# Kernel optimization log

Measured on AMD Instinct MI355X. Metric: run time of the kernel, lower is better.

The kernel has to match this reference:

```python
import jax, jax.numpy as jnp
import numpy as np
import math

B, S, D, H = 2, 2048, 1024, 32
HD = D // H  # head_dim = 32
NEG = -1e9


def setup_inputs() -> dict:
    key = jax.random.key(0)
    ks = jax.random.split(key, 6)
    x = jax.random.normal(ks[0], (B, S, D), dtype=jnp.float32)
    # additive causal mask: 0 on/below diagonal, -1e9 above
    causal = jnp.tril(jnp.ones((S, S), dtype=bool))
    mask = jnp.where(causal, 0.0, NEG).astype(jnp.float32)[None, None]
    # SSMax-style per-query-position log-length scale
    section_log_len = jnp.log(jnp.arange(1, S + 1, dtype=jnp.float32) + 1.0).reshape(1, 1, S, 1)
    sc = 1.0 / math.sqrt(D)
    wq = jax.random.normal(ks[1], (D, D), dtype=jnp.float32) * sc
    wk = jax.random.normal(ks[2], (D, D), dtype=jnp.float32) * sc
    wv = jax.random.normal(ks[3], (D, D), dtype=jnp.float32) * sc
    wo = jax.random.normal(ks[4], (D, D), dtype=jnp.float32) * sc
    seq_scale = jnp.ones((1, H, 1, 1), dtype=jnp.float32)
    return {"x": x, "mask": mask, "section_log_len": section_log_len,
            "wq": wq, "wk": wk, "wv": wv, "wo": wo, "seq_scale": seq_scale}


def reference(x, mask, section_log_len, wq, wk, wv, wo, seq_scale):
    bsz, seqlen, dim = x.shape
    # projections (torch Linear: y = x @ W.T); split heads -> [b, h, s, hd]
    q = (x @ wq.T).reshape(bsz, seqlen, H, HD).transpose(0, 2, 1, 3)
    k = (x @ wk.T).reshape(bsz, seqlen, H, HD).transpose(0, 2, 1, 3)
    v = (x @ wv.T).reshape(bsz, seqlen, H, HD).transpose(0, 2, 1, 3)
    # n_kv_heads == n_heads, so repeat_kv is identity
    scores = jnp.einsum('bhqd,bhkd->bhqk', q, k) / math.sqrt(HD)
    scores = scores * (section_log_len * seq_scale)  # SSMax per-head learned scale
    scores = scores + mask
    probs = jax.nn.softmax(scores.astype(jnp.float32), axis=-1).astype(q.dtype)
    out = jnp.einsum('bhqk,bhkd->bhqd', probs, v)
    out = out.transpose(0, 2, 1, 3).reshape(bsz, seqlen, dim)
    return out @ wo.T
```

## Files before the change

kernel.cpp:

```cpp
#include <hip/hip_runtime.h>
#include <hip/hip_bf16.h>

typedef __bf16 bf16_t;
typedef bf16_t bf16x8 __attribute__((ext_vector_type(8)));
typedef float f32x4 __attribute__((ext_vector_type(4)));

#define NB 2
#define SEQ 2048
#define DIM 1024
#define NH 32
#define HDIM 32

#define LDA 40

static __device__ __forceinline__ f32x4 mfma16(bf16x8 a, bf16x8 b, f32x4 c) {
    return __builtin_amdgcn_mfma_f32_16x16x32_bf16(a, b, c, 0, 0, 0);
}

static __device__ __forceinline__ void load_lds16(const bf16_t* g, bf16_t* l) {
    __builtin_amdgcn_global_load_lds(
        (const __attribute__((address_space(1))) void*)(g),
        (__attribute__((address_space(3))) void*)(l), 16, 0, 0);
}

__global__ __launch_bounds__(256)
void cvt_f32_bf16(const float* __restrict__ s0, bf16_t* __restrict__ d0, int n0,
                  const float* __restrict__ s1, bf16_t* __restrict__ d1, int n1,
                  const float* __restrict__ s2, bf16_t* __restrict__ d2, int n2,
                  const float* __restrict__ s3, bf16_t* __restrict__ d3, int n3,
                  const float* __restrict__ s4, bf16_t* __restrict__ d4, int n4) {
    const int stride = gridDim.x * blockDim.x;
    const int tid = blockIdx.x * blockDim.x + threadIdx.x;
    const float* src[5] = {s0, s1, s2, s3, s4};
    bf16_t* dst[5] = {d0, d1, d2, d3, d4};
    const int n[5] = {n0, n1, n2, n3, n4};
#pragma unroll
    for (int r = 0; r < 5; r++) {
        const int nv = n[r] >> 2;
        for (int i = tid; i < nv; i += stride) {
            float4 v = ((const float4*)src[r])[i];
            bf16_t o[4] = {(bf16_t)v.x, (bf16_t)v.y, (bf16_t)v.z, (bf16_t)v.w};
            *(uint2*)(dst[r] + i * 4) = *(const uint2*)o;
        }
    }
}

template <int EPI, int BM>
__global__ __launch_bounds__(256)
void gemm_pipe(const bf16_t* __restrict__ A, const bf16_t* __restrict__ W,
               float* __restrict__ Cf, bf16_t* __restrict__ qb,
               bf16_t* __restrict__ kb, bf16_t* __restrict__ vtb,
               const float* __restrict__ slen, const float* __restrict__ ss) {
    constexpr int MI = BM / 32;
    __shared__ alignas(16) bf16_t As[2 * BM * 32];
    __shared__ alignas(16) bf16_t Bs[2 * 128 * 32];
    const int t = threadIdx.x;
    const int lane = t & 63, wave = t >> 6;
    const int lane16 = lane & 15, quad = lane >> 4;
    const int wm = (wave >> 1) * (BM / 2), wn = (wave & 1) * 64;
    const int id = blockIdx.x;
    int m0, n0g;
    if (EPI == 1) {
        const int xcd = id & 7, slot = id >> 3;
        m0 = (xcd + 8 * (slot & 3)) * 128;
        n0g = (slot >> 2) * 128;
    } else {
        const int xcd = id & 7, slot = id >> 3;
        m0 = (xcd + 8 * (slot & 7)) * 64;
        n0g = (slot >> 3) * 128;
    }
    const int tr = t >> 2;
    const int tc = (t & 3) * 8;
    const bf16_t* ga = A + (m0 + tr) * DIM + tc;
    const bf16_t* gb = W + (n0g + tr) * DIM + tc;
    const bool vseg = (EPI == 1) && (n0g >= 2048);

    f32x4 acc[MI][4];
#pragma unroll
    for (int i = 0; i < MI; i++)
#pragma unroll
        for (int j = 0; j < 4; j++) acc[i][j] = f32x4{0.f, 0.f, 0.f, 0.f};

    auto stage = [&](int k0, int buf) {
        bf16_t* a_dst = As + buf * (BM * 32) + (t & 192) * 8;
        bf16_t* b_dst = Bs + buf * 4096 + (t & 192) * 8;
        load_lds16(ga + k0, a_dst);
        if (BM == 128) load_lds16(ga + 64 * DIM + k0, a_dst + 2048);
        load_lds16(gb + k0, b_dst);
        load_lds16(gb + 64 * DIM + k0, b_dst + 2048);
    };
    auto compute = [&](int buf) {
        bf16x8 af[MI], bfr[4];
#pragma unroll
        for (int mi = 0; mi < MI; mi++)
            af[mi] = *(const bf16x8*)(As + buf * (BM * 32) +
                                      (wm + mi * 16 + lane16) * 32 + quad * 8);
#pragma unroll
        for (int ni = 0; ni < 4; ni++)
            bfr[ni] = *(const bf16x8*)(Bs + buf * 4096 +
                                       (wn + ni * 16 + lane16) * 32 + quad * 8);
        if (vseg) {
#pragma unroll
            for (int mi = 0; mi < MI; mi++)
#pragma unroll
                for (int ni = 0; ni < 4; ni++)
                    acc[mi][ni] = mfma16(bfr[ni], af[mi], acc[mi][ni]);
        } else {
#pragma unroll
            for (int mi = 0; mi < MI; mi++)
#pragma unroll
                for (int ni = 0; ni < 4; ni++)
                    acc[mi][ni] = mfma16(af[mi], bfr[ni], acc[mi][ni]);
        }
    };

    stage(0, 0);
#pragma unroll
    for (int k0 = 0; k0 < DIM; k0 += 32) {
        const int cur = (k0 >> 5) & 1;
        if (k0 + 32 < DIM) {
            stage(k0 + 32, cur ^ 1);
            if (BM == 128)
                asm volatile("s_waitcnt vmcnt(4)" ::: "memory");
            else
                asm volatile("s_waitcnt vmcnt(3)" ::: "memory");
        } else {
            asm volatile("s_waitcnt vmcnt(0)" ::: "memory");
        }
        asm volatile("s_barrier" ::: "memory");
        compute(cur);
        if (k0 + 32 < DIM) {
            asm volatile("s_waitcnt lgkmcnt(0)" ::: "memory");
            asm volatile("s_barrier" ::: "memory");
        }
    }

    if (EPI == 0) {
#pragma unroll
        for (int mi = 0; mi < MI; mi++)
#pragma unroll
            for (int ni = 0; ni < 4; ni++)
#pragma unroll
                for (int r = 0; r < 4; r++) {
                    int row = m0 + wm + mi * 16 + quad * 4 + r;
                    int col = n0g + wn + ni * 16 + lane16;
                    Cf[row * DIM + col] = acc[mi][ni][r];
                }
    } else if (!vseg) {
        const bool isq = (n0g < 1024);
        bf16_t* dst = isq ? qb : kb;
        const int nb = n0g & 1023;
#pragma unroll
        for (int mi = 0; mi < MI; mi++)
#pragma unroll
            for (int ni = 0; ni < 4; ni++) {
                const int h = ((nb + wn) >> 5) + (ni >> 1);
                const float hscale =
                    isq ? ss[h] * 0.17677669529663687f : 0.f;
#pragma unroll
                for (int r = 0; r < 4; r++) {
                    int m = m0 + wm + mi * 16 + quad * 4 + r;
                    int nl = nb + wn + ni * 16 + lane16;
                    int b = m >> 11, s = m & (SEQ - 1);
                    int d = nl & 31;
                    float v = acc[mi][ni][r];
                    if (isq) v *= slen[s] * hscale;
                    dst[(((b * NH + h) << 11) + s) * 32 + d] = (bf16_t)v;
                }
            }
    } else {
        const int nb = n0g & 1023;
#pragma unroll
        for (int mi = 0; mi < MI; mi++)
#pragma unroll
            for (int ni = 0; ni < 4; ni++)
#pragma unroll
                for (int r = 0; r < 4; r++) {
                    int nl = nb + wn + ni * 16 + quad * 4 + r;
                    int m = m0 + wm + mi * 16 + lane16;
                    int b = m >> 11, s = m & (SEQ - 1);
                    int h = nl >> 5, d = nl & 31;
                    vtb[(((b * NH + h) << 5) + d) * SEQ + s] = (bf16_t)acc[mi][ni][r];
                }
    }
}

__global__ __launch_bounds__(256)
void attn_fwd(const bf16_t* __restrict__ q, const bf16_t* __restrict__ k,
              const bf16_t* __restrict__ vt, bf16_t* __restrict__ out) {
    __shared__ alignas(16) bf16_t pscr[4][32 * LDA];
    const int t = threadIdx.x;
    const int lane = t & 63, wave = t >> 6;
    const int lane16 = lane & 15, quad = lane >> 4;
    const int gw = blockIdx.x * 4 + wave;
    const int idx = gw & 63;
    const int qt = (idx & 1) ? (63 - (idx >> 1)) : (idx >> 1);
    const int h = (gw >> 6) & (NH - 1);
    const int b = gw >> 11;
    const int q0 = qt * 32;
    const bf16_t* qh = q + (b * NH + h) * SEQ * HDIM;
    const bf16_t* kh = k + (b * NH + h) * SEQ * HDIM;
    const bf16_t* vth = vt + (b * NH + h) * HDIM * SEQ;
    bf16_t* psw = pscr[wave];

    bf16x8 qf[2];
    qf[0] = *(const bf16x8*)(qh + (q0 + lane16) * HDIM + quad * 8);
    qf[1] = *(const bf16x8*)(qh + (q0 + 16 + lane16) * HDIM + quad * 8);

    f32x4 o[2][2];
    float lrow[2][4];
#pragma unroll
    for (int mi = 0; mi < 2; mi++)
#pragma unroll
        for (int r = 0; r < 4; r++) lrow[mi][r] = 0.f;
#pragma unroll
    for (int mi = 0; mi < 2; mi++)
#pragma unroll
        for (int ni = 0; ni < 2; ni++) o[mi][ni] = f32x4{0.f, 0.f, 0.f, 0.f};

    const bf16_t* kp0 = kh + (2 * lane16) * HDIM + quad * 8;
    const bf16_t* vp0 = vth + lane16 * SEQ + quad * 8;
    const bf16_t* vp1 = vth + (16 + lane16) * SEQ + quad * 8;

    auto process = [&](bf16x8 kf0, bf16x8 kf1, int kv, bool domask) {
        const f32x4 zz = f32x4{0.f, 0.f, 0.f, 0.f};
        f32x4 sc[2][2];
        sc[0][0] = mfma16(qf[0], kf0, zz);
        sc[0][1] = mfma16(qf[0], kf1, zz);
        sc[1][0] = mfma16(qf[1], kf0, zz);
        sc[1][1] = mfma16(qf[1], kf1, zz);
        bf16x8 vf0 = *(const bf16x8*)(vp0 + kv);
        bf16x8 vf1 = *(const bf16x8*)(vp1 + kv);
#pragma unroll
        for (int mi = 0; mi < 2; mi++)
#pragma unroll
            for (int r = 0; r < 4; r++) {
                float p0 = __expf(sc[mi][0][r]);
                float p1 = __expf(sc[mi][1][r]);
                if (domask) {
                    const int rowloc = mi * 16 + quad * 4 + r;
                    if (2 * lane16 > rowloc) p0 = 0.f;
                    if (2 * lane16 + 1 > rowloc) p1 = 0.f;
                }
                lrow[mi][r] += p0 + p1;
                bf16_t pb[2] = {(bf16_t)p0, (bf16_t)p1};
                *(unsigned int*)(psw + (mi * 16 + quad * 4 + r) * LDA +
                                 2 * lane16) = *(const unsigned int*)pb;
            }
        asm volatile("s_waitcnt lgkmcnt(0)" ::: "memory");
        bf16x8 pf0 = *(const bf16x8*)(psw + lane16 * LDA + quad * 8);
        bf16x8 pf1 = *(const bf16x8*)(psw + (16 + lane16) * LDA + quad * 8);
        o[0][0] = mfma16(pf0, vf0, o[0][0]);
        o[0][1] = mfma16(pf0, vf1, o[0][1]);
        o[1][0] = mfma16(pf1, vf0, o[1][0]);
        o[1][1] = mfma16(pf1, vf1, o[1][1]);
    };

    bf16x8 kc0 = *(const bf16x8*)(kp0);
    bf16x8 kc1 = *(const bf16x8*)(kp0 + HDIM);
    for (int kv = 0; kv < q0; kv += 32) {
        bf16x8 kn0 = *(const bf16x8*)(kp0 + (kv + 32) * HDIM);
        bf16x8 kn1 = *(const bf16x8*)(kp0 + (kv + 32) * HDIM + HDIM);
        process(kc0, kc1, kv, false);
        kc0 = kn0;
        kc1 = kn1;
    }
    process(kc0, kc1, q0, true);

#pragma unroll
    for (int mi = 0; mi < 2; mi++)
#pragma unroll
        for (int r = 0; r < 4; r++) {
            float l = lrow[mi][r];
#pragma unroll
            for (int off = 1; off < 16; off <<= 1) l += __shfl_xor(l, off);
            float inv = 1.0f / l;
            int qi = q0 + mi * 16 + quad * 4 + r;
            bf16_t* ob = out + (b * SEQ + qi) * DIM + h * HDIM;
#pragma unroll
            for (int ni = 0; ni < 2; ni++)
                ob[ni * 16 + lane16] = (bf16_t)(o[mi][ni][r] * inv);
        }
}

extern "C" void kernel_launch(void* const* d_in, const int* in_sizes, int n_in,
                              void* d_out, int out_size, void* d_ws, size_t ws_size,
                              hipStream_t stream) {
    const float* x = (const float*)d_in[0];
    const float* slen = (const float*)d_in[2];
    const float* wq = (const float*)d_in[3];
    const float* wk = (const float*)d_in[4];
    const float* wv = (const float*)d_in[5];
    const float* wo = (const float*)d_in[6];
    const float* ss = (const float*)d_in[7];

    const size_t ELEMS = (size_t)NB * SEQ * DIM;
    const size_t WELEMS = (size_t)DIM * DIM;
    bf16_t* xb = (bf16_t*)d_ws;
    bf16_t* abuf = xb;
    bf16_t* wqkvb = xb + ELEMS;
    bf16_t* wob = wqkvb + 3 * WELEMS;
    bf16_t* qbuf = wob + WELEMS;
    bf16_t* vtbuf = qbuf + ELEMS;
    bf16_t* kbuf = (bf16_t*)d_out;

    dim3 blk(256);
    cvt_f32_bf16<<<dim3(1024), blk, 0, stream>>>(
        x, xb, (int)ELEMS, wq, wqkvb, (int)WELEMS, wk, wqkvb + WELEMS,
        (int)WELEMS, wv, wqkvb + 2 * WELEMS, (int)WELEMS, wo, wob, (int)WELEMS);

    gemm_pipe<1, 128><<<dim3(768), blk, 0, stream>>>(
        xb, wqkvb, nullptr, qbuf, kbuf, vtbuf, slen, ss);
    attn_fwd<<<dim3(NB * NH * (SEQ / 32) / 4), blk, 0, stream>>>(
        qbuf, kbuf, vtbuf, abuf);
    gemm_pipe<0, 64><<<dim3(512), blk, 0, stream>>>(
        abuf, wob, (float*)d_out, nullptr, nullptr, nullptr, nullptr, nullptr);
}
```

Baseline: 214.0 us.

## Split attention KV range across wave pairs, use exp2 with folded log2e scale

Each query tile is now handled by two waves that split the causal KV range in half and combine their partial outputs and row sums through shared memory, which doubles the grid and shortens the longest per-wave loop. The log2(e) factor is folded into the Q scaling so the softmax can use the raw v_exp_f32 instruction instead of __expf. s_setprio is raised around the MFMA blocks to favour matrix issue. The cost is an extra block-wide barrier and an LDS reduction, and half the waves sit idle during the final normalisation.

```diff
diff --git a/kernel.cpp b/kernel.cpp
--- a/kernel.cpp
+++ b/kernel.cpp
@@ -15,6 +15,12 @@
 
 static __device__ __forceinline__ f32x4 mfma16(bf16x8 a, bf16x8 b, f32x4 c) {
     return __builtin_amdgcn_mfma_f32_16x16x32_bf16(a, b, c, 0, 0, 0);
+}
+
+static __device__ __forceinline__ float fexp2(float x) {
+    float r;
+    asm("v_exp_f32 %0, %1" : "=v"(r) : "v"(x));
+    return r;
 }
 
 static __device__ __forceinline__ void load_lds16(const bf16_t* g, bf16_t* l) {
@@ -156,7 +162,8 @@
             for (int ni = 0; ni < 4; ni++) {
                 const int h = ((nb + wn) >> 5) + (ni >> 1);
                 const float hscale =
-                    isq ? ss[h] * 0.17677669529663687f : 0.f;
+                    isq ? ss[h] * (0.17677669529663687f * 1.4426950408889634f)
+                        : 0.f;
 #pragma unroll
                 for (int r = 0; r < 4; r++) {
                     int m = m0 + wm + mi * 16 + quad * 4 + r;
@@ -189,14 +196,16 @@
 void attn_fwd(const bf16_t* __restrict__ q, const bf16_t* __restrict__ k,
               const bf16_t* __restrict__ vt, bf16_t* __restrict__ out) {
     __shared__ alignas(16) bf16_t pscr[4][32 * LDA];
+    __shared__ float comb[2][64][25];
     const int t = threadIdx.x;
     const int lane = t & 63, wave = t >> 6;
     const int lane16 = lane & 15, quad = lane >> 4;
-    const int gw = blockIdx.x * 4 + wave;
-    const int idx = gw & 63;
-    const int qt = (idx & 1) ? (63 - (idx >> 1)) : (idx >> 1);
-    const int h = (gw >> 6) & (NH - 1);
-    const int b = gw >> 11;
+    const int pairid = wave >> 1;
+    const int whalf = wave & 1;
+    const int s0i = blockIdx.x >> 6;
+    const int bh = blockIdx.x & 63;
+    const int h = bh & (NH - 1), b = bh >> 5;
+    const int qt = 63 - 2 * s0i - pairid;
     const int q0 = qt * 32;
     const bf16_t* qh = q + (b * NH + h) * SEQ * HDIM;
     const bf16_t* kh = k + (b * NH + h) * SEQ * HDIM;
@@ -225,18 +234,20 @@
     auto process = [&](bf16x8 kf0, bf16x8 kf1, int kv, bool domask) {
         const f32x4 zz = f32x4{0.f, 0.f, 0.f, 0.f};
         f32x4 sc[2][2];
+        __builtin_amdgcn_s_setprio(1);
         sc[0][0] = mfma16(qf[0], kf0, zz);
         sc[0][1] = mfma16(qf[0], kf1, zz);
         sc[1][0] = mfma16(qf[1], kf0, zz);
         sc[1][1] = mfma16(qf[1], kf1, zz);
+        __builtin_amdgcn_s_setprio(0);
         bf16x8 vf0 = *(const bf16x8*)(vp0 + kv);
         bf16x8 vf1 = *(const bf16x8*)(vp1 + kv);
 #pragma unroll
         for (int mi = 0; mi < 2; mi++)
 #pragma unroll
             for (int r = 0; r < 4; r++) {
-                float p0 = __expf(sc[mi][0][r]);
-                float p1 = __expf(sc[mi][1][r]);
+                float p0 = fexp2(sc[mi][0][r]);
+                float p1 = fexp2(sc[mi][1][r]);
                 if (domask) {
                     const int rowloc = mi * 16 + quad * 4 + r;
                     if (2 * lane16 > rowloc) p0 = 0.f;
@@ -250,22 +261,60 @@
         asm volatile("s_waitcnt lgkmcnt(0)" ::: "memory");
         bf16x8 pf0 = *(const bf16x8*)(psw + lane16 * LDA + quad * 8);
         bf16x8 pf1 = *(const bf16x8*)(psw + (16 + lane16) * LDA + quad * 8);
+        __builtin_amdgcn_s_setprio(1);
         o[0][0] = mfma16(pf0, vf0, o[0][0]);
         o[0][1] = mfma16(pf0, vf1, o[0][1]);
         o[1][0] = mfma16(pf1, vf0, o[1][0]);
         o[1][1] = mfma16(pf1, vf1, o[1][1]);
+        __builtin_amdgcn_s_setprio(0);
     };
 
-    bf16x8 kc0 = *(const bf16x8*)(kp0);
-    bf16x8 kc1 = *(const bf16x8*)(kp0 + HDIM);
-    for (int kv = 0; kv < q0; kv += 32) {
-        bf16x8 kn0 = *(const bf16x8*)(kp0 + (kv + 32) * HDIM);
-        bf16x8 kn1 = *(const bf16x8*)(kp0 + (kv + 32) * HDIM + HDIM);
-        process(kc0, kc1, kv, false);
-        kc0 = kn0;
-        kc1 = kn1;
-    }
-    process(kc0, kc1, q0, true);
+    const int nh = (qt + 1) >> 1;
+    const int kvb = whalf ? 0 : nh * 32;
+    const int kve = whalf ? nh * 32 - 32 : q0;
+    if (kve >= kvb) {
+        bf16x8 kc0 = *(const bf16x8*)(kp0 + kvb * HDIM);
+        bf16x8 kc1 = *(const bf16x8*)(kp0 + kvb * HDIM + HDIM);
+        for (int kv = kvb; kv < kve; kv += 32) {
+            bf16x8 kn0 = *(const bf16x8*)(kp0 + (kv + 32) * HDIM);
+            bf16x8 kn1 = *(const bf16x8*)(kp0 + (kv + 32) * HDIM + HDIM);
+            process(kc0, kc1, kv, false);
+            kc0 = kn0;
+            kc1 = kn1;
+        }
+        process(kc0, kc1, kve, kve == q0);
+    }
+
+    if (whalf) {
+        float* c = comb[pairid][lane];
+#pragma unroll
+        for (int mi = 0; mi < 2; mi++)
+#pragma unroll
+            for (int ni = 0; ni < 2; ni++)
+#pragma unroll
+                for (int r = 0; r < 4; r++)
+                    c[(mi * 2 + ni) * 4 + r] = o[mi][ni][r];
+#pragma unroll
+        for (int mi = 0; mi < 2; mi++)
+#pragma unroll
+            for (int r = 0; r < 4; r++) c[16 + mi * 4 + r] = lrow[mi][r];
+    }
+    __syncthreads();
+    if (whalf) return;
+    {
+        const float* c = comb[pairid][lane];
+#pragma unroll
+        for (int mi = 0; mi < 2; mi++)
+#pragma unroll
+            for (int ni = 0; ni < 2; ni++)
+#pragma unroll
+                for (int r = 0; r < 4; r++)
+                    o[mi][ni][r] += c[(mi * 2 + ni) * 4 + r];
+#pragma unroll
+        for (int mi = 0; mi < 2; mi++)
+#pragma unroll
+            for (int r = 0; r < 4; r++) lrow[mi][r] += c[16 + mi * 4 + r];
+    }
 
 #pragma unroll
     for (int mi = 0; mi < 2; mi++)
@@ -311,7 +360,7 @@
 
     gemm_pipe<1, 128><<<dim3(768), blk, 0, stream>>>(
         xb, wqkvb, nullptr, qbuf, kbuf, vtbuf, slen, ss);
-    attn_fwd<<<dim3(NB * NH * (SEQ / 32) / 4), blk, 0, stream>>>(
+    attn_fwd<<<dim3(NB * NH * (SEQ / 32) / 2), blk, 0, stream>>>(
         qbuf, kbuf, vtbuf, abuf);
     gemm_pipe<0, 64><<<dim3(512), blk, 0, stream>>>(
         abuf, wob, (float*)d_out, nullptr, nullptr, nullptr, nullptr, nullptr);
```

Result: slower. 219.7 us (+2.7%).

## Software-pipeline attention loop with double-buffered P scratch and MFMA row sums

Applied to the files above, without the earlier changes.

Restructures the attention inner loop so the QK MFMAs for block i overlap with the exp and LDS write for block i and the PV MFMAs for block i-1, using two LDS P buffers per wave. This removes the explicit lgkmcnt wait between writing and reading P. Row sums are now computed by an MFMA against a ones vector instead of scalar adds plus a shuffle reduction. exp is done with a raw v_exp_f32 (base 2), with log2(e) folded into the Q scale, and s_setprio hints are placed around the MFMA groups. Without the explicit wait, LDS ordering relies on the compiler's own waitcnt insertion, and the row sums now come from bf16-rounded probabilities.

```diff
diff --git a/kernel.cpp b/kernel.cpp
--- a/kernel.cpp
+++ b/kernel.cpp
@@ -15,6 +15,12 @@
 
 static __device__ __forceinline__ f32x4 mfma16(bf16x8 a, bf16x8 b, f32x4 c) {
     return __builtin_amdgcn_mfma_f32_16x16x32_bf16(a, b, c, 0, 0, 0);
+}
+
+static __device__ __forceinline__ float fexp2(float x) {
+    float r;
+    asm("v_exp_f32 %0, %1" : "=v"(r) : "v"(x));
+    return r;
 }
 
 static __device__ __forceinline__ void load_lds16(const bf16_t* g, bf16_t* l) {
@@ -156,7 +162,8 @@
             for (int ni = 0; ni < 4; ni++) {
                 const int h = ((nb + wn) >> 5) + (ni >> 1);
                 const float hscale =
-                    isq ? ss[h] * 0.17677669529663687f : 0.f;
+                    isq ? ss[h] * (0.17677669529663687f * 1.4426950408889634f)
+                        : 0.f;
 #pragma unroll
                 for (int r = 0; r < 4; r++) {
                     int m = m0 + wm + mi * 16 + quad * 4 + r;
@@ -188,7 +195,7 @@
 __global__ __launch_bounds__(256)
 void attn_fwd(const bf16_t* __restrict__ q, const bf16_t* __restrict__ k,
               const bf16_t* __restrict__ vt, bf16_t* __restrict__ out) {
-    __shared__ alignas(16) bf16_t pscr[4][32 * LDA];
+    __shared__ alignas(16) bf16_t pscr[4][2][32 * LDA];
     const int t = threadIdx.x;
     const int lane = t & 63, wave = t >> 6;
     const int lane16 = lane & 15, quad = lane >> 4;
@@ -201,85 +208,128 @@
     const bf16_t* qh = q + (b * NH + h) * SEQ * HDIM;
     const bf16_t* kh = k + (b * NH + h) * SEQ * HDIM;
     const bf16_t* vth = vt + (b * NH + h) * HDIM * SEQ;
-    bf16_t* psw = pscr[wave];
+
+    bf16_t* wbase0 = pscr[wave][0] + quad * 4 * LDA + 2 * lane16;
+    bf16_t* wbase1 = pscr[wave][1] + quad * 4 * LDA + 2 * lane16;
+    const bf16_t* rbase0 = pscr[wave][0] + lane16 * LDA + quad * 8;
+    const bf16_t* rbase1 = pscr[wave][1] + lane16 * LDA + quad * 8;
 
     bf16x8 qf[2];
     qf[0] = *(const bf16x8*)(qh + (q0 + lane16) * HDIM + quad * 8);
     qf[1] = *(const bf16x8*)(qh + (q0 + 16 + lane16) * HDIM + quad * 8);
 
-    f32x4 o[2][2];
-    float lrow[2][4];
-#pragma unroll
-    for (int mi = 0; mi < 2; mi++)
-#pragma unroll
-        for (int r = 0; r < 4; r++) lrow[mi][r] = 0.f;
-#pragma unroll
-    for (int mi = 0; mi < 2; mi++)
+    bf16x8 ones;
+#pragma unroll
+    for (int j = 0; j < 8; j++) ones[j] = (bf16_t)1.0f;
+
+    f32x4 o[2][2], ol[2], sc[2][2];
+#pragma unroll
+    for (int mi = 0; mi < 2; mi++) {
+        ol[mi] = f32x4{0.f, 0.f, 0.f, 0.f};
 #pragma unroll
         for (int ni = 0; ni < 2; ni++) o[mi][ni] = f32x4{0.f, 0.f, 0.f, 0.f};
+    }
 
     const bf16_t* kp0 = kh + (2 * lane16) * HDIM + quad * 8;
     const bf16_t* vp0 = vth + lane16 * SEQ + quad * 8;
     const bf16_t* vp1 = vth + (16 + lane16) * SEQ + quad * 8;
 
-    auto process = [&](bf16x8 kf0, bf16x8 kf1, int kv, bool domask) {
-        const f32x4 zz = f32x4{0.f, 0.f, 0.f, 0.f};
-        f32x4 sc[2][2];
-        sc[0][0] = mfma16(qf[0], kf0, zz);
-        sc[0][1] = mfma16(qf[0], kf1, zz);
-        sc[1][0] = mfma16(qf[1], kf0, zz);
-        sc[1][1] = mfma16(qf[1], kf1, zz);
-        bf16x8 vf0 = *(const bf16x8*)(vp0 + kv);
-        bf16x8 vf1 = *(const bf16x8*)(vp1 + kv);
+    const f32x4 zz = f32x4{0.f, 0.f, 0.f, 0.f};
+    bf16x8 kc0, kc1, pf0, pf1, vprev0, vprev1;
+
+    auto qk = [&]() {
+        __builtin_amdgcn_s_setprio(1);
+        sc[0][0] = mfma16(qf[0], kc0, zz);
+        sc[0][1] = mfma16(qf[0], kc1, zz);
+        sc[1][0] = mfma16(qf[1], kc0, zz);
+        sc[1][1] = mfma16(qf[1], kc1, zz);
+        __builtin_amdgcn_s_setprio(0);
+    };
+    auto ldp = [&](const bf16_t* rb) {
+        pf0 = *(const bf16x8*)(rb);
+        pf1 = *(const bf16x8*)(rb + 16 * LDA);
+    };
+    auto expw = [&](bf16_t* wb, bool domask) {
 #pragma unroll
         for (int mi = 0; mi < 2; mi++)
 #pragma unroll
             for (int r = 0; r < 4; r++) {
-                float p0 = __expf(sc[mi][0][r]);
-                float p1 = __expf(sc[mi][1][r]);
+                float p0 = fexp2(sc[mi][0][r]);
+                float p1 = fexp2(sc[mi][1][r]);
                 if (domask) {
                     const int rowloc = mi * 16 + quad * 4 + r;
                     if (2 * lane16 > rowloc) p0 = 0.f;
                     if (2 * lane16 + 1 > rowloc) p1 = 0.f;
                 }
-                lrow[mi][r] += p0 + p1;
                 bf16_t pb[2] = {(bf16_t)p0, (bf16_t)p1};
-                *(unsigned int*)(psw + (mi * 16 + quad * 4 + r) * LDA +
-                                 2 * lane16) = *(const unsigned int*)pb;
+                *(unsigned int*)(wb + (mi * 16 + r) * LDA) =
+                    *(const unsigned int*)pb;
             }
-        asm volatile("s_waitcnt lgkmcnt(0)" ::: "memory");
-        bf16x8 pf0 = *(const bf16x8*)(psw + lane16 * LDA + quad * 8);
-        bf16x8 pf1 = *(const bf16x8*)(psw + (16 + lane16) * LDA + quad * 8);
-        o[0][0] = mfma16(pf0, vf0, o[0][0]);
-        o[0][1] = mfma16(pf0, vf1, o[0][1]);
-        o[1][0] = mfma16(pf1, vf0, o[1][0]);
-        o[1][1] = mfma16(pf1, vf1, o[1][1]);
-    };
-
-    bf16x8 kc0 = *(const bf16x8*)(kp0);
-    bf16x8 kc1 = *(const bf16x8*)(kp0 + HDIM);
-    for (int kv = 0; kv < q0; kv += 32) {
+    };
+    auto pv = [&]() {
+        __builtin_amdgcn_s_setprio(1);
+        o[0][0] = mfma16(pf0, vprev0, o[0][0]);
+        o[0][1] = mfma16(pf0, vprev1, o[0][1]);
+        o[1][0] = mfma16(pf1, vprev0, o[1][0]);
+        o[1][1] = mfma16(pf1, vprev1, o[1][1]);
+        ol[0] = mfma16(pf0, ones, ol[0]);
+        ol[1] = mfma16(pf1, ones, ol[1]);
+        __builtin_amdgcn_s_setprio(0);
+    };
+
+    const int nb = qt + 1;
+
+    kc0 = *(const bf16x8*)(kp0);
+    kc1 = *(const bf16x8*)(kp0 + HDIM);
+    qk();
+    vprev0 = *(const bf16x8*)(vp0);
+    vprev1 = *(const bf16x8*)(vp1);
+    if (nb > 1) {
+        kc0 = *(const bf16x8*)(kp0 + 32 * HDIM);
+        kc1 = *(const bf16x8*)(kp0 + 32 * HDIM + HDIM);
+    }
+    expw(wbase0, nb == 1);
+
+    for (int i = 1; i < nb - 1; i++) {
+        const int kv = i << 5;
+        qk();
+        bf16x8 vc0 = *(const bf16x8*)(vp0 + kv);
+        bf16x8 vc1 = *(const bf16x8*)(vp1 + kv);
         bf16x8 kn0 = *(const bf16x8*)(kp0 + (kv + 32) * HDIM);
         bf16x8 kn1 = *(const bf16x8*)(kp0 + (kv + 32) * HDIM + HDIM);
-        process(kc0, kc1, kv, false);
+        ldp(((i - 1) & 1) ? rbase1 : rbase0);
+        expw((i & 1) ? wbase1 : wbase0, false);
+        pv();
         kc0 = kn0;
         kc1 = kn1;
-    }
-    process(kc0, kc1, q0, true);
+        vprev0 = vc0;
+        vprev1 = vc1;
+    }
+
+    if (nb > 1) {
+        const int kv = (nb - 1) << 5;
+        qk();
+        bf16x8 vc0 = *(const bf16x8*)(vp0 + kv);
+        bf16x8 vc1 = *(const bf16x8*)(vp1 + kv);
+        ldp(((nb - 2) & 1) ? rbase1 : rbase0);
+        expw(((nb - 1) & 1) ? wbase1 : wbase0, true);
+        pv();
+        vprev0 = vc0;
+        vprev1 = vc1;
+    }
+
+    ldp(((nb - 1) & 1) ? rbase1 : rbase0);
+    pv();
 
 #pragma unroll
     for (int mi = 0; mi < 2; mi++)
 #pragma unroll
         for (int r = 0; r < 4; r++) {
-            float l = lrow[mi][r];
-#pragma unroll
-            for (int off = 1; off < 16; off <<= 1) l += __shfl_xor(l, off);
-            float inv = 1.0f / l;
+            float inv = 1.0f / ol[mi][r];
             int qi = q0 + mi * 16 + quad * 4 + r;
             bf16_t* ob = out + (b * SEQ + qi) * DIM + h * HDIM;
-#pragma unroll
-            for (int ni = 0; ni < 2; ni++)
-                ob[ni * 16 + lane16] = (bf16_t)(o[mi][ni][r] * inv);
+            ob[lane16] = (bf16_t)(o[mi][0][r] * inv);
+            ob[16 + lane16] = (bf16_t)(o[mi][1][r] * inv);
         }
 }
 
```

After: 214.4 us. About the same (+0.2%).
